# Optimization experiments

Measured on AMD Instinct MI355X. Metric: run time of the kernel, lower is better.

## Reference

```python
import jax, jax.numpy as jnp
import numpy as np

N_NODES = 50000
N_EDGES = 800000
IN_C, HID, OUT_C = 128, 128, 16
N_GRAPHS = 128


def setup_inputs() -> dict:
    key = jax.random.key(0)
    ks = jax.random.split(key, 8)
    x = jax.random.normal(ks[0], (N_NODES, IN_C), dtype=jnp.float32)
    edge_index = jax.random.randint(ks[1], (2, N_EDGES), 0, N_NODES, dtype=jnp.int64)
    batch = jnp.sort(jax.random.randint(ks[2], (N_NODES,), 0, N_GRAPHS, dtype=jnp.int64))
    s1 = 1.0 / np.sqrt(IN_C)
    s2 = 1.0 / np.sqrt(HID)
    W1 = jax.random.normal(ks[3], (IN_C, HID), dtype=jnp.float32) * s1
    b1 = jnp.zeros((HID,), dtype=jnp.float32)
    W2 = jax.random.normal(ks[4], (HID, HID), dtype=jnp.float32) * s2
    b2 = jnp.zeros((HID,), dtype=jnp.float32)
    Wfc = jax.random.normal(ks[5], (HID, OUT_C), dtype=jnp.float32) * s2
    bfc = jnp.zeros((OUT_C,), dtype=jnp.float32)
    return {"x": x, "edge_index": edge_index, "batch": batch,
            "W1": W1, "b1": b1, "W2": W2, "b2": b2, "Wfc": Wfc, "bfc": bfc}


def _gcn_conv(x, W, b, src, dst, deg_inv_sqrt, n_nodes):
    # linear transform first (PyG order), then normalized sparse aggregation
    h = x @ W  # [N, H]
    norm = deg_inv_sqrt[src] * deg_inv_sqrt[dst]  # [E+N] (self-loops appended)
    msgs = h[src] * norm[:, None]  # [E+N, H] dominant gather
    agg = jax.ops.segment_sum(msgs, dst, num_segments=n_nodes)
    return agg + b


def reference(x, edge_index, batch, W1, b1, W2, b2, Wfc, bfc):
    n = x.shape[0]
    loops = jnp.arange(n, dtype=edge_index.dtype)
    src = jnp.concatenate([edge_index[0], loops])
    dst = jnp.concatenate([edge_index[1], loops])
    # symmetric normalization with self-loops: deg computed on dst
    deg = jax.ops.segment_sum(jnp.ones_like(src, dtype=x.dtype), dst, num_segments=n)
    deg_inv_sqrt = jnp.where(deg > 0, jax.lax.rsqrt(jnp.maximum(deg, 1.0)), 0.0)

    h = jax.nn.relu(_gcn_conv(x, W1, b1, src, dst, deg_inv_sqrt, n))
    h = jax.nn.relu(_gcn_conv(h, W2, b2, src, dst, deg_inv_sqrt, n))

    # global mean pool over graph ids
    sums = jax.ops.segment_sum(h, batch, num_segments=N_GRAPHS)
    counts = jax.ops.segment_sum(jnp.ones((n,), dtype=h.dtype), batch, num_segments=N_GRAPHS)
    pooled = sums / jnp.maximum(counts, 1.0)[:, None]  # [G, H]

    logits = pooled @ Wfc + bfc  # [G, OUT_C]
    return jax.nn.log_softmax(logits, axis=1)
```

## Files before the change

kernel.cpp:

```cpp
#include <hip/hip_runtime.h>

#define N_NODES  50000
#define N_EDGES  800000
#define HID      128
#define OUT_C    16
#define N_GRAPHS 128
#define MAXDEG   64
#define NSLICE   6250
#define EPB      1024
#define FILLB    6256
#define GEMMB    782
#define AGB      3125
#define PAD      136

typedef __attribute__((ext_vector_type(8))) short bf16x8;
typedef __attribute__((ext_vector_type(4))) float f32x4;
typedef __attribute__((ext_vector_type(8))) unsigned short us8;
typedef __attribute__((ext_vector_type(4))) unsigned short us4;

__device__ __forceinline__ unsigned short f2bf(float f) {
  unsigned u = __float_as_uint(f);
  u += 0x7fffu + ((u >> 16) & 1u);
  return (unsigned short)(u >> 16);
}

__device__ __forceinline__ void gemm_compute_store(
    unsigned short* sA, const float* __restrict__ W,
    unsigned short* __restrict__ T, int base) {
  const int tid = threadIdx.x;
  const int lane = tid & 63;
  const int w = tid >> 6;
  const int l15 = lane & 15;
  const int quad = lane >> 4;
  __syncthreads();

  f32x4 acc[4][2];
#pragma unroll
  for (int nt = 0; nt < 4; ++nt)
#pragma unroll
    for (int c = 0; c < 2; ++c) acc[nt][c] = (f32x4)(0.f);

  const int ct0 = w * 2;
  const int ncol = ct0 * 16 + l15;
#pragma unroll
  for (int ks = 0; ks < 4; ++ks) {
    const int koff = ks * 32 + quad * 8;
    bf16x8 a[4], bfr[2];
#pragma unroll
    for (int c = 0; c < 2; ++c) {
      const float* wp = W + (size_t)koff * HID + ncol + c * 16;
#pragma unroll
      for (int j = 0; j < 8; ++j) bfr[c][j] = (short)f2bf(wp[(size_t)j * HID]);
    }
#pragma unroll
    for (int nt = 0; nt < 4; ++nt)
      a[nt] = *(const bf16x8*)(sA + (nt * 16 + l15) * PAD + koff);
#pragma unroll
    for (int nt = 0; nt < 4; ++nt)
#pragma unroll
      for (int c = 0; c < 2; ++c)
        acc[nt][c] = __builtin_amdgcn_mfma_f32_16x16x32_bf16(a[nt], bfr[c], acc[nt][c], 0, 0, 0);
  }
  __syncthreads();

#pragma unroll
  for (int nt = 0; nt < 4; ++nt)
#pragma unroll
    for (int c = 0; c < 2; ++c)
#pragma unroll
      for (int r = 0; r < 4; ++r)
        sA[(nt * 16 + quad * 4 + r) * PAD + (ct0 + c) * 16 + l15] = f2bf(acc[nt][c][r]);
  __syncthreads();
#pragma unroll
  for (int i = 0; i < 4; ++i) {
    int idx = tid + i * 256;
    int nrow = idx >> 4;
    int col = (idx & 15) * 8;
    int node = base + nrow;
    if (node < N_NODES)
      *(us8*)(T + (size_t)node * HID + col) = *(const us8*)(sA + nrow * PAD + col);
  }
}

__device__ __forceinline__ void stage_a_f32(unsigned short* sA,
                                            const float* __restrict__ H, int base) {
#pragma unroll
  for (int i = 0; i < 8; ++i) {
    int idx = threadIdx.x + i * 256;
    int nrow = idx >> 5;
    int c4 = (idx & 31) * 4;
    float4 v = make_float4(0.f, 0.f, 0.f, 0.f);
    int node = base + nrow;
    if (node < N_NODES) v = *(const float4*)(H + (size_t)node * HID + c4);
    us4 b;
    b.x = f2bf(v.x); b.y = f2bf(v.y); b.z = f2bf(v.z); b.w = f2bf(v.w);
    *(us4*)(sA + nrow * PAD + c4) = b;
  }
}

__global__ __launch_bounds__(256) void mega_kernel(
    const int* __restrict__ src, const int* __restrict__ dst,
    int* __restrict__ deg, unsigned short* __restrict__ ell,
    const int* __restrict__ batch, int* __restrict__ start,
    const float* __restrict__ x, const float* __restrict__ W1,
    unsigned short* __restrict__ T) {
  __shared__ unsigned short sA[64 * PAD];
  int b = blockIdx.x;
  if (b < FILLB + GEMMB) {
    if (b % 9 == 8) {
      const int base = (b / 9) * 64;
      stage_a_f32(sA, x, base);
      gemm_compute_store(sA, W1, T, base);
    } else {
      const int fi = b - (b + 1) / 9;
      const int slice = fi & 7;
      const int e0 = (fi >> 3) * EPB;
      const int e1 = min(e0 + EPB, N_EDGES);
      const unsigned lo = slice * NSLICE;
      for (int e = e0 + threadIdx.x; e < e1; e += 256) {
        int d = __builtin_nontemporal_load(dst + e);
        if ((unsigned)(d - lo) < (unsigned)NSLICE) {
          int p = atomicAdd(&deg[d], 1);
          if (p < MAXDEG) ell[(d << 6) + p] = (unsigned short)src[e];
        }
      }
    }
  } else {
    int t = threadIdx.x;
    if (t <= N_GRAPHS) {
      int lo = 0, hi = N_NODES;
      while (lo < hi) {
        int mid = (lo + hi) >> 1;
        if (batch[mid] < t) lo = mid + 1; else hi = mid;
      }
      start[t] = lo;
    }
  }
}

__device__ __forceinline__ void agg_node_pack(
    int node, int lane, const unsigned int* __restrict__ Tb,
    const unsigned short* __restrict__ ell, const int* __restrict__ deg,
    unsigned int* __restrict__ ellw,
    float bx, float by, float& ox, float& oy) {
  int dn = deg[node];
  float dd = rsqrtf((float)dn + 1.0f);
  unsigned sv = Tb[(size_t)node * 64 + lane];
  float wself = dd * dd;
  float ax = __int_as_float(sv << 16) * wself;
  float ay = __int_as_float(sv & 0xffff0000u) * wself;
  int m = min(dn, MAXDEG);
  int s0 = node << 6;
  int sidx = 0; float wv = 0.f;
  if (lane < m) {
    sidx = (int)ell[s0 + lane];
    wv = rsqrtf((float)deg[sidx] + 1.0f) * dd;
    unsigned short hw = __builtin_bit_cast(unsigned short, (_Float16)wv);
    ellw[s0 + lane] = (unsigned)sidx | ((unsigned)hw << 16);
  }
  const int mt = (m + 7) & ~7;
  for (int j = 0; j < mt; j += 8) {
#pragma unroll
    for (int q = 0; q < 8; ++q) {
      int s = __builtin_amdgcn_readlane(sidx, j + q);
      float w = __int_as_float(__builtin_amdgcn_readlane(__float_as_int(wv), j + q));
      unsigned t = Tb[(size_t)s * 64 + lane];
      ax += w * __int_as_float(t << 16);
      ay += w * __int_as_float(t & 0xffff0000u);
    }
  }
  ox = fmaxf(ax + bx, 0.f);
  oy = fmaxf(ay + by, 0.f);
}

__global__ __launch_bounds__(1024) void agg_gemm_kernel(
    const unsigned int* __restrict__ Tb, const unsigned short* __restrict__ ell,
    const int* __restrict__ deg, const float* __restrict__ bias,
    const float* __restrict__ W, unsigned int* __restrict__ ellw,
    unsigned short* __restrict__ T2) {
  __shared__ unsigned short sA[16 * PAD];
  const int tid = threadIdx.x;
  const int lane = tid & 63;
  const int w = tid >> 6;
  const int l15 = lane & 15;
  const int quad = lane >> 4;
  const int base = blockIdx.x * 16;

  {
    float2 b = ((const float2*)bias)[lane];
    float ox, oy;
    agg_node_pack(base + w, lane, Tb, ell, deg, ellw, b.x, b.y, ox, oy);
    *(unsigned*)(sA + w * PAD + lane * 2) =
        (unsigned)f2bf(ox) | ((unsigned)f2bf(oy) << 16);
  }
  __syncthreads();

  f32x4 acc = (f32x4)(0.f);
  if (w < 8) {
    const int ncol = w * 16 + l15;
#pragma unroll
    for (int ks = 0; ks < 4; ++ks) {
      const int koff = ks * 32 + quad * 8;
      bf16x8 a = *(const bf16x8*)(sA + l15 * PAD + koff);
      bf16x8 bfr;
      const float* wp = W + (size_t)koff * HID + ncol;
#pragma unroll
      for (int j = 0; j < 8; ++j) bfr[j] = (short)f2bf(wp[(size_t)j * HID]);
      acc = __builtin_amdgcn_mfma_f32_16x16x32_bf16(a, bfr, acc, 0, 0, 0);
    }
  }
  __syncthreads();
  if (w < 8) {
#pragma unroll
    for (int r = 0; r < 4; ++r)
      sA[(quad * 4 + r) * PAD + w * 16 + l15] = f2bf(acc[r]);
  }
  __syncthreads();
  if (tid < 256) {
    int nrow = tid >> 4;
    int col = (tid & 15) * 8;
    *(us8*)(T2 + (size_t)(base + nrow) * HID + col) = *(const us8*)(sA + nrow * PAD + col);
  }
}

__global__ __launch_bounds__(256) void aggregate_kernel(
    const unsigned int* __restrict__ Tb, const unsigned int* __restrict__ ellw,
    const int* __restrict__ deg, const float* __restrict__ bias,
    unsigned int* __restrict__ Hb) {
  int wid = (blockIdx.x * 256 + threadIdx.x) >> 6;
  int lane = threadIdx.x & 63;
  int n0 = wid * 2;
  if (n0 >= N_NODES) return;
  int n1 = n0 + 1;
  float2 b = ((const float2*)bias)[lane];
  int d0 = deg[n0], d1 = deg[n1];
  float r0 = rsqrtf((float)d0 + 1.f), r1 = rsqrtf((float)d1 + 1.f);
  unsigned sv0 = Tb[(size_t)n0 * 64 + lane];
  unsigned sv1 = Tb[(size_t)n1 * 64 + lane];
  float ax0 = __int_as_float(sv0 << 16) * (r0 * r0);
  float ay0 = __int_as_float(sv0 & 0xffff0000u) * (r0 * r0);
  float ax1 = __int_as_float(sv1 << 16) * (r1 * r1);
  float ay1 = __int_as_float(sv1 & 0xffff0000u) * (r1 * r1);
  int m0 = min(d0, MAXDEG), m1 = min(d1, MAXDEG);
  unsigned pw0 = 0, pw1 = 0;
  if (lane < m0) pw0 = ellw[(n0 << 6) + lane];
  if (lane < m1) pw1 = ellw[(n1 << 6) + lane];
  const int mt = (max(m0, m1) + 7) & ~7;
  for (int j = 0; j < mt; j += 8) {
#pragma unroll
    for (int q = 0; q < 8; ++q) {
      unsigned v0 = (unsigned)__builtin_amdgcn_readlane((int)pw0, j + q);
      unsigned v1 = (unsigned)__builtin_amdgcn_readlane((int)pw1, j + q);
      unsigned t0 = Tb[(size_t)(v0 & 0xffffu) * 64 + lane];
      unsigned t1 = Tb[(size_t)(v1 & 0xffffu) * 64 + lane];
      float w0 = (float)__builtin_bit_cast(_Float16, (unsigned short)(v0 >> 16));
      float w1 = (float)__builtin_bit_cast(_Float16, (unsigned short)(v1 >> 16));
      ax0 += w0 * __int_as_float(t0 << 16);
      ay0 += w0 * __int_as_float(t0 & 0xffff0000u);
      ax1 += w1 * __int_as_float(t1 << 16);
      ay1 += w1 * __int_as_float(t1 & 0xffff0000u);
    }
  }
  Hb[(size_t)n0 * 64 + lane] =
      (unsigned)f2bf(fmaxf(ax0 + b.x, 0.f)) |
      ((unsigned)f2bf(fmaxf(ay0 + b.y, 0.f)) << 16);
  Hb[(size_t)n1 * 64 + lane] =
      (unsigned)f2bf(fmaxf(ax1 + b.x, 0.f)) |
      ((unsigned)f2bf(fmaxf(ay1 + b.y, 0.f)) << 16);
}

__global__ __launch_bounds__(256) void pool_partial_kernel(
    const unsigned int* __restrict__ Hb, const int* __restrict__ start,
    float* __restrict__ pooled) {
  __shared__ float2 red[4][64];
  int g = blockIdx.x >> 2;
  int chunk = blockIdx.x & 3;
  int n0 = start[g], n1 = start[g + 1];
  int lane = threadIdx.x & 63, w = threadIdx.x >> 6;
  float ax = 0.f, ay = 0.f;
  for (int n = n0 + chunk * 4 + w; n < n1; n += 16) {
    unsigned h = Hb[(size_t)n * 64 + lane];
    ax += __int_as_float(h << 16);
    ay += __int_as_float(h & 0xffff0000u);
  }
  red[w][lane] = make_float2(ax, ay);
  __syncthreads();
  if (threadIdx.x < 64) {
    float2 a = red[0][lane], b = red[1][lane], c = red[2][lane], d = red[3][lane];
    atomicAdd(&pooled[g * HID + lane * 2],     a.x + b.x + c.x + d.x);
    atomicAdd(&pooled[g * HID + lane * 2 + 1], a.y + b.y + c.y + d.y);
  }
}

__global__ __launch_bounds__(64) void head_kernel(
    const float* __restrict__ pooled, const int* __restrict__ start,
    const float* __restrict__ Wfc, const float* __restrict__ bfc,
    float* __restrict__ out) {
  int g = blockIdx.x;
  int lane = threadIdx.x;
  int o = lane & 15;
  float inv = 1.0f / fmaxf((float)(start[g + 1] - start[g]), 1.0f);
  float part = 0.f;
  for (int k = (lane >> 4); k < HID; k += 4)
    part += pooled[g * HID + k] * inv * Wfc[k * OUT_C + o];
  part += __shfl_xor(part, 16);
  part += __shfl_xor(part, 32);
  float logit = part + bfc[o];
  float m = logit;
#pragma unroll
  for (int d = 8; d >= 1; d >>= 1) m = fmaxf(m, __shfl_xor(m, d, 16));
  float e = __expf(logit - m);
  float s = e;
#pragma unroll
  for (int d = 8; d >= 1; d >>= 1) s += __shfl_xor(s, d, 16);
  float r = logit - m - __logf(s);
  if (lane < 16) out[g * OUT_C + o] = r;
}

extern "C" void kernel_launch(void* const* d_in, const int* in_sizes, int n_in,
                              void* d_out, int out_size, void* d_ws, size_t ws_size,
                              hipStream_t stream) {
  const float* x    = (const float*)d_in[0];
  const int*   ei   = (const int*)d_in[1];
  const int*   batch= (const int*)d_in[2];
  const float* W1   = (const float*)d_in[3];
  const float* b1   = (const float*)d_in[4];
  const float* W2   = (const float*)d_in[5];
  const float* b2   = (const float*)d_in[6];
  const float* Wfc  = (const float*)d_in[7];
  const float* bfc  = (const float*)d_in[8];
  float* out = (float*)d_out;
  const int* src = ei;
  const int* dst = ei + N_EDGES;

  char* p = (char*)d_ws;
  auto alloc = [&](size_t bytes) { char* r = p; p += (bytes + 255) & ~255ull; return r; };
  int*   degI   = (int*)alloc((size_t)N_NODES * 4);
  float* pooled = (float*)alloc((size_t)N_GRAPHS * HID * 4);
  int*   start  = (int*)alloc((N_GRAPHS + 1) * 4);
  unsigned short* ell = (unsigned short*)alloc((size_t)N_NODES * MAXDEG * 2);
  unsigned int*   ellw= (unsigned int*)alloc((size_t)N_NODES * MAXDEG * 4);
  unsigned short* T   = (unsigned short*)alloc((size_t)N_NODES * HID * 2);
  unsigned short* T2  = (unsigned short*)alloc((size_t)N_NODES * HID * 2);
  unsigned short* Hb  = (unsigned short*)alloc((size_t)N_NODES * HID * 2);

  hipMemsetAsync(degI, 0, ((size_t)N_NODES * 4 + 255 & ~255ull) +
                          (size_t)N_GRAPHS * HID * 4, stream);

  int agg_blocks = (N_NODES / 2 * 64 + 255) / 256;

  mega_kernel<<<FILLB + GEMMB + 1, 256, 0, stream>>>(src, dst, degI, ell,
                                                     batch, start, x, W1, T);
  agg_gemm_kernel<<<AGB, 1024, 0, stream>>>((const unsigned int*)T, ell, degI,
                                            b1, W2, ellw, T2);
  aggregate_kernel<<<agg_blocks, 256, 0, stream>>>((const unsigned int*)T2, ellw, degI, b2,
                                                   (unsigned int*)Hb);
  pool_partial_kernel<<<N_GRAPHS * 4, 256, 0, stream>>>((const unsigned int*)Hb, start,
                                                        pooled);
  head_kernel<<<N_GRAPHS, 64, 0, stream>>>(pooled, start, Wfc, bfc, out);
}
```

Measured before the change: 237.6 us.

## Process four nodes per wave in aggregation and regroup fill/GEMM block interleave

The final aggregation kernel now handles four nodes per wavefront instead of two, so each wave keeps more independent gathers in flight, and the grid is cut to match. The fused fill/GEMM kernel's block mapping changes from one GEMM block every nine to groups of 64 fill blocks followed by 8 GEMM blocks, with tail handling. The x staging load becomes a nontemporal load. The risks are higher register pressure from four accumulators, extra wasted work when neighbour degrees vary within a wave, and fewer waves for scheduling.

Result: faster. 225.6 us (-5.0%).

```diff
diff --git a/kernel.cpp b/kernel.cpp
--- a/kernel.cpp
+++ b/kernel.cpp
@@ -13,6 +13,10 @@
 #define AGB      3125
 #define PAD      136
 
+#define GRP      72
+#define NGRP     97
+#define GB0      6984
+
 typedef __attribute__((ext_vector_type(8))) short bf16x8;
 typedef __attribute__((ext_vector_type(4))) float f32x4;
 typedef __attribute__((ext_vector_type(8))) unsigned short us8;
@@ -89,9 +93,10 @@
     int idx = threadIdx.x + i * 256;
     int nrow = idx >> 5;
     int c4 = (idx & 31) * 4;
-    float4 v = make_float4(0.f, 0.f, 0.f, 0.f);
+    f32x4 v = (f32x4)(0.f);
     int node = base + nrow;
-    if (node < N_NODES) v = *(const float4*)(H + (size_t)node * HID + c4);
+    if (node < N_NODES)
+      v = __builtin_nontemporal_load((const f32x4*)(H + (size_t)node * HID + c4));
     us4 b;
     b.x = f2bf(v.x); b.y = f2bf(v.y); b.z = f2bf(v.z); b.w = f2bf(v.w);
     *(us4*)(sA + nrow * PAD + c4) = b;
@@ -105,26 +110,33 @@
     const float* __restrict__ x, const float* __restrict__ W1,
     unsigned short* __restrict__ T) {
   __shared__ unsigned short sA[64 * PAD];
-  int b = blockIdx.x;
-  if (b < FILLB + GEMMB) {
-    if (b % 9 == 8) {
-      const int base = (b / 9) * 64;
-      stage_a_f32(sA, x, base);
-      gemm_compute_store(sA, W1, T, base);
-    } else {
-      const int fi = b - (b + 1) / 9;
-      const int slice = fi & 7;
-      const int e0 = (fi >> 3) * EPB;
-      const int e1 = min(e0 + EPB, N_EDGES);
-      const unsigned lo = slice * NSLICE;
-      for (int e = e0 + threadIdx.x; e < e1; e += 256) {
-        int d = __builtin_nontemporal_load(dst + e);
-        if ((unsigned)(d - lo) < (unsigned)NSLICE) {
-          int p = atomicAdd(&deg[d], 1);
-          if (p < MAXDEG) ell[(d << 6) + p] = (unsigned short)src[e];
-        }
+  const int b = blockIdx.x;
+  int fi = -1, gi = -1;
+  if (b < GB0) {
+    const int g = b / GRP, r = b % GRP;
+    if (r < 64) fi = g * 64 + r;
+    else        gi = g * 8 + (r - 64);
+  } else {
+    const int r = b - GB0;
+    if (r < 48)      fi = NGRP * 64 + r;
+    else if (r < 54) gi = NGRP * 8 + (r - 48);
+  }
+  if (fi >= 0) {
+    const int slice = fi & 7;
+    const int e0 = (fi >> 3) * EPB;
+    const int e1 = min(e0 + EPB, N_EDGES);
+    const unsigned lo = slice * NSLICE;
+    for (int e = e0 + threadIdx.x; e < e1; e += 256) {
+      int d = __builtin_nontemporal_load(dst + e);
+      if ((unsigned)(d - lo) < (unsigned)NSLICE) {
+        int p = atomicAdd(&deg[d], 1);
+        if (p < MAXDEG) ell[(d << 6) + p] = (unsigned short)src[e];
       }
     }
+  } else if (gi >= 0) {
+    const int base = gi * 64;
+    stage_a_f32(sA, x, base);
+    gemm_compute_store(sA, W1, T, base);
   } else {
     int t = threadIdx.x;
     if (t <= N_GRAPHS) {
@@ -229,44 +241,43 @@
     unsigned int* __restrict__ Hb) {
   int wid = (blockIdx.x * 256 + threadIdx.x) >> 6;
   int lane = threadIdx.x & 63;
-  int n0 = wid * 2;
+  int n0 = wid * 4;
   if (n0 >= N_NODES) return;
-  int n1 = n0 + 1;
   float2 b = ((const float2*)bias)[lane];
-  int d0 = deg[n0], d1 = deg[n1];
-  float r0 = rsqrtf((float)d0 + 1.f), r1 = rsqrtf((float)d1 + 1.f);
-  unsigned sv0 = Tb[(size_t)n0 * 64 + lane];
-  unsigned sv1 = Tb[(size_t)n1 * 64 + lane];
-  float ax0 = __int_as_float(sv0 << 16) * (r0 * r0);
-  float ay0 = __int_as_float(sv0 & 0xffff0000u) * (r0 * r0);
-  float ax1 = __int_as_float(sv1 << 16) * (r1 * r1);
-  float ay1 = __int_as_float(sv1 & 0xffff0000u) * (r1 * r1);
-  int m0 = min(d0, MAXDEG), m1 = min(d1, MAXDEG);
-  unsigned pw0 = 0, pw1 = 0;
-  if (lane < m0) pw0 = ellw[(n0 << 6) + lane];
-  if (lane < m1) pw1 = ellw[(n1 << 6) + lane];
-  const int mt = (max(m0, m1) + 7) & ~7;
+  float ax[4], ay[4];
+  unsigned pw[4];
+  int m_max = 0;
+#pragma unroll
+  for (int k = 0; k < 4; ++k) {
+    int n = n0 + k;
+    int d = deg[n];
+    float r = rsqrtf((float)d + 1.f);
+    unsigned sv = Tb[(size_t)n * 64 + lane];
+    ax[k] = __int_as_float(sv << 16) * (r * r);
+    ay[k] = __int_as_float(sv & 0xffff0000u) * (r * r);
+    int m = min(d, MAXDEG);
+    m_max = max(m_max, m);
+    pw[k] = (lane < m) ? ellw[(n << 6) + lane] : 0u;
+  }
+  const int mt = (m_max + 7) & ~7;
   for (int j = 0; j < mt; j += 8) {
 #pragma unroll
     for (int q = 0; q < 8; ++q) {
-      unsigned v0 = (unsigned)__builtin_amdgcn_readlane((int)pw0, j + q);
-      unsigned v1 = (unsigned)__builtin_amdgcn_readlane((int)pw1, j + q);
-      unsigned t0 = Tb[(size_t)(v0 & 0xffffu) * 64 + lane];
-      unsigned t1 = Tb[(size_t)(v1 & 0xffffu) * 64 + lane];
-      float w0 = (float)__builtin_bit_cast(_Float16, (unsigned short)(v0 >> 16));
-      float w1 = (float)__builtin_bit_cast(_Float16, (unsigned short)(v1 >> 16));
-      ax0 += w0 * __int_as_float(t0 << 16);
-      ay0 += w0 * __int_as_float(t0 & 0xffff0000u);
-      ax1 += w1 * __int_as_float(t1 << 16);
-      ay1 += w1 * __int_as_float(t1 & 0xffff0000u);
-    }
-  }
-  Hb[(size_t)n0 * 64 + lane] =
-      (unsigned)f2bf(fmaxf(ax0 + b.x, 0.f)) |
-      ((unsigned)f2bf(fmaxf(ay0 + b.y, 0.f)) << 16);
-  Hb[(size_t)n1 * 64 + lane] =
-      (unsigned)f2bf(fmaxf(ax1 + b.x, 0.f)) |
-      ((unsigned)f2bf(fmaxf(ay1 + b.y, 0.f)) << 16);
+#pragma unroll
+      for (int k = 0; k < 4; ++k) {
+        unsigned v = (unsigned)__builtin_amdgcn_readlane((int)pw[k], j + q);
+        unsigned t = Tb[(size_t)(v & 0xffffu) * 64 + lane];
+        float w = (float)__builtin_bit_cast(_Float16, (unsigned short)(v >> 16));
+        ax[k] += w * __int_as_float(t << 16);
+        ay[k] += w * __int_as_float(t & 0xffff0000u);
+      }
+    }
+  }
+#pragma unroll
+  for (int k = 0; k < 4; ++k)
+    Hb[(size_t)(n0 + k) * 64 + lane] =
+        (unsigned)f2bf(fmaxf(ax[k] + b.x, 0.f)) |
+        ((unsigned)f2bf(fmaxf(ay[k] + b.y, 0.f)) << 16);
 }
 
 __global__ __launch_bounds__(256) void pool_partial_kernel(
@@ -347,14 +358,12 @@
   hipMemsetAsync(degI, 0, ((size_t)N_NODES * 4 + 255 & ~255ull) +
                           (size_t)N_GRAPHS * HID * 4, stream);
 
-  int agg_blocks = (N_NODES / 2 * 64 + 255) / 256;
-
-  mega_kernel<<<FILLB + GEMMB + 1, 256, 0, stream>>>(src, dst, degI, ell,
-                                                     batch, start, x, W1, T);
+  mega_kernel<<<GB0 + 55, 256, 0, stream>>>(src, dst, degI, ell,
+                                            batch, start, x, W1, T);
   agg_gemm_kernel<<<AGB, 1024, 0, stream>>>((const unsigned int*)T, ell, degI,
                                             b1, W2, ellw, T2);
-  aggregate_kernel<<<agg_blocks, 256, 0, stream>>>((const unsigned int*)T2, ellw, degI, b2,
-                                                   (unsigned int*)Hb);
+  aggregate_kernel<<<AGB, 256, 0, stream>>>((const unsigned int*)T2, ellw, degI, b2,
+                                            (unsigned int*)Hb);
   pool_partial_kernel<<<N_GRAPHS * 4, 256, 0, stream>>>((const unsigned int*)Hb, start,
                                                         pooled);
   head_kernel<<<N_GRAPHS, 64, 0, stream>>>(pooled, start, Wfc, bfc, out);
```

## Fuse mean-pool into second aggregation via atomics and regroup mega-kernel block schedule

Applied to the files above, without the earlier changes.

The second aggregation kernel now atomically adds each node's ReLU output straight into the per-graph pooled sums. This drops the bf16 Hb intermediate buffer and the separate pool_partial kernel. The mega kernel's block-to-work mapping changes from a 1-in-9 GEMM interleave to groups of 64 fill blocks plus 8 GEMM blocks, and the x loads use nontemporal hints. The cost is about 6.4M float atomics landing on only 128x128 addresses, with heavy contention because batch is sorted and consecutive nodes share a graph.

New measurement: 284.6 us. 1.2x slower.

```diff
diff --git a/kernel.cpp b/kernel.cpp
--- a/kernel.cpp
+++ b/kernel.cpp
@@ -8,10 +8,12 @@
 #define MAXDEG   64
 #define NSLICE   6250
 #define EPB      1024
-#define FILLB    6256
-#define GEMMB    782
 #define AGB      3125
 #define PAD      136
+
+#define GRP      72
+#define NGRP     97
+#define GB0      6984
 
 typedef __attribute__((ext_vector_type(8))) short bf16x8;
 typedef __attribute__((ext_vector_type(4))) float f32x4;
@@ -89,9 +91,10 @@
     int idx = threadIdx.x + i * 256;
     int nrow = idx >> 5;
     int c4 = (idx & 31) * 4;
-    float4 v = make_float4(0.f, 0.f, 0.f, 0.f);
+    f32x4 v = (f32x4)(0.f);
     int node = base + nrow;
-    if (node < N_NODES) v = *(const float4*)(H + (size_t)node * HID + c4);
+    if (node < N_NODES)
+      v = __builtin_nontemporal_load((const f32x4*)(H + (size_t)node * HID + c4));
     us4 b;
     b.x = f2bf(v.x); b.y = f2bf(v.y); b.z = f2bf(v.z); b.w = f2bf(v.w);
     *(us4*)(sA + nrow * PAD + c4) = b;
@@ -105,26 +108,33 @@
     const float* __restrict__ x, const float* __restrict__ W1,
     unsigned short* __restrict__ T) {
   __shared__ unsigned short sA[64 * PAD];
-  int b = blockIdx.x;
-  if (b < FILLB + GEMMB) {
-    if (b % 9 == 8) {
-      const int base = (b / 9) * 64;
-      stage_a_f32(sA, x, base);
-      gemm_compute_store(sA, W1, T, base);
-    } else {
-      const int fi = b - (b + 1) / 9;
-      const int slice = fi & 7;
-      const int e0 = (fi >> 3) * EPB;
-      const int e1 = min(e0 + EPB, N_EDGES);
-      const unsigned lo = slice * NSLICE;
-      for (int e = e0 + threadIdx.x; e < e1; e += 256) {
-        int d = __builtin_nontemporal_load(dst + e);
-        if ((unsigned)(d - lo) < (unsigned)NSLICE) {
-          int p = atomicAdd(&deg[d], 1);
-          if (p < MAXDEG) ell[(d << 6) + p] = (unsigned short)src[e];
-        }
+  const int b = blockIdx.x;
+  int fi = -1, gi = -1;
+  if (b < GB0) {
+    const int g = b / GRP, r = b % GRP;
+    if (r < 64) fi = g * 64 + r;
+    else        gi = g * 8 + (r - 64);
+  } else {
+    const int r = b - GB0;
+    if (r < 48)      fi = NGRP * 64 + r;
+    else if (r < 54) gi = NGRP * 8 + (r - 48);
+  }
+  if (fi >= 0) {
+    const int slice = fi & 7;
+    const int e0 = (fi >> 3) * EPB;
+    const int e1 = min(e0 + EPB, N_EDGES);
+    const unsigned lo = slice * NSLICE;
+    for (int e = e0 + threadIdx.x; e < e1; e += 256) {
+      int d = __builtin_nontemporal_load(dst + e);
+      if ((unsigned)(d - lo) < (unsigned)NSLICE) {
+        int p = atomicAdd(&deg[d], 1);
+        if (p < MAXDEG) ell[(d << 6) + p] = (unsigned short)src[e];
       }
     }
+  } else if (gi >= 0) {
+    const int base = gi * 64;
+    stage_a_f32(sA, x, base);
+    gemm_compute_store(sA, W1, T, base);
   } else {
     int t = threadIdx.x;
     if (t <= N_GRAPHS) {
@@ -226,7 +236,7 @@
 __global__ __launch_bounds__(256) void aggregate_kernel(
     const unsigned int* __restrict__ Tb, const unsigned int* __restrict__ ellw,
     const int* __restrict__ deg, const float* __restrict__ bias,
-    unsigned int* __restrict__ Hb) {
+    const int* __restrict__ batch, float* __restrict__ pooled) {
   int wid = (blockIdx.x * 256 + threadIdx.x) >> 6;
   int lane = threadIdx.x & 63;
   int n0 = wid * 2;
@@ -261,35 +271,13 @@
       ay1 += w1 * __int_as_float(t1 & 0xffff0000u);
     }
   }
-  Hb[(size_t)n0 * 64 + lane] =
-      (unsigned)f2bf(fmaxf(ax0 + b.x, 0.f)) |
-      ((unsigned)f2bf(fmaxf(ay0 + b.y, 0.f)) << 16);
-  Hb[(size_t)n1 * 64 + lane] =
-      (unsigned)f2bf(fmaxf(ax1 + b.x, 0.f)) |
-      ((unsigned)f2bf(fmaxf(ay1 + b.y, 0.f)) << 16);
-}
-
-__global__ __launch_bounds__(256) void pool_partial_kernel(
-    const unsigned int* __restrict__ Hb, const int* __restrict__ start,
-    float* __restrict__ pooled) {
-  __shared__ float2 red[4][64];
-  int g = blockIdx.x >> 2;
-  int chunk = blockIdx.x & 3;
-  int n0 = start[g], n1 = start[g + 1];
-  int lane = threadIdx.x & 63, w = threadIdx.x >> 6;
-  float ax = 0.f, ay = 0.f;
-  for (int n = n0 + chunk * 4 + w; n < n1; n += 16) {
-    unsigned h = Hb[(size_t)n * 64 + lane];
-    ax += __int_as_float(h << 16);
-    ay += __int_as_float(h & 0xffff0000u);
-  }
-  red[w][lane] = make_float2(ax, ay);
-  __syncthreads();
-  if (threadIdx.x < 64) {
-    float2 a = red[0][lane], b = red[1][lane], c = red[2][lane], d = red[3][lane];
-    atomicAdd(&pooled[g * HID + lane * 2],     a.x + b.x + c.x + d.x);
-    atomicAdd(&pooled[g * HID + lane * 2 + 1], a.y + b.y + c.y + d.y);
-  }
+  int g0 = batch[n0], g1 = batch[n1];
+  float* p0 = pooled + g0 * HID + lane * 2;
+  float* p1 = pooled + g1 * HID + lane * 2;
+  atomicAdd(p0,     fmaxf(ax0 + b.x, 0.f));
+  atomicAdd(p0 + 1, fmaxf(ay0 + b.y, 0.f));
+  atomicAdd(p1,     fmaxf(ax1 + b.x, 0.f));
+  atomicAdd(p1 + 1, fmaxf(ay1 + b.y, 0.f));
 }
 
 __global__ __launch_bounds__(64) void head_kernel(
@@ -342,20 +330,17 @@
   unsigned int*   ellw= (unsigned int*)alloc((size_t)N_NODES * MAXDEG * 4);
   unsigned short* T   = (unsigned short*)alloc((size_t)N_NODES * HID * 2);
   unsigned short* T2  = (unsigned short*)alloc((size_t)N_NODES * HID * 2);
-  unsigned short* Hb  = (unsigned short*)alloc((size_t)N_NODES * HID * 2);
 
   hipMemsetAsync(degI, 0, ((size_t)N_NODES * 4 + 255 & ~255ull) +
                           (size_t)N_GRAPHS * HID * 4, stream);
 
   int agg_blocks = (N_NODES / 2 * 64 + 255) / 256;
 
-  mega_kernel<<<FILLB + GEMMB + 1, 256, 0, stream>>>(src, dst, degI, ell,
-                                                     batch, start, x, W1, T);
+  mega_kernel<<<GB0 + 55, 256, 0, stream>>>(src, dst, degI, ell,
+                                            batch, start, x, W1, T);
   agg_gemm_kernel<<<AGB, 1024, 0, stream>>>((const unsigned int*)T, ell, degI,
                                             b1, W2, ellw, T2);
   aggregate_kernel<<<agg_blocks, 256, 0, stream>>>((const unsigned int*)T2, ellw, degI, b2,
-                                                   (unsigned int*)Hb);
-  pool_partial_kernel<<<N_GRAPHS * 4, 256, 0, stream>>>((const unsigned int*)Hb, start,
-                                                        pooled);
+                                                   batch, pooled);
   head_kernel<<<N_GRAPHS, 64, 0, stream>>>(pooled, start, Wfc, bfc, out);
 }
```
